# Performance work log

Hardware: AMD Instinct MI355X
Metric: run time of the kernel (lower is better)

Reference implementation:

```python
import jax, jax.numpy as jnp
import numpy as np

N = 50000
E_RAND = 800000
IN, HID, OUT = 128, 64, 40
HEADS = (2, 1, 1)
NEG_SLOPE = 0.2


def setup_inputs() -> dict:
    key = jax.random.key(0)
    ks = jax.random.split(key, 16)
    # random edges with src != dst, then append self-loops (remove+add_self_loop)
    src_r = jax.random.randint(ks[0], (E_RAND,), 0, N)
    off = jax.random.randint(ks[1], (E_RAND,), 1, N)
    dst_r = (src_r + off) % N
    loops = jnp.arange(N)
    src = jnp.concatenate([src_r, loops]).astype(jnp.int64)
    dst = jnp.concatenate([dst_r, loops]).astype(jnp.int64)
    in_feat = jax.random.normal(ks[2], (N, IN), dtype=jnp.float32)

    def lin(k, fan_in, fan_out):
        return jax.random.normal(k, (fan_in, fan_out), dtype=jnp.float32) / np.sqrt(fan_in)

    H0, H1, H2 = HEADS
    # layer 0: in=IN, out=HID, heads=H0
    W0 = lin(ks[3], IN, H0 * HID)
    al0 = jax.random.normal(ks[4], (H0, HID), dtype=jnp.float32) * 0.1
    ar0 = jax.random.normal(ks[5], (H0, HID), dtype=jnp.float32) * 0.1
    b0 = jnp.zeros((H0 * HID,), dtype=jnp.float32)
    # layer 1: in=HID*H0, out=HID, heads=H1
    W1 = lin(ks[6], HID * H0, H1 * HID)
    al1 = jax.random.normal(ks[7], (H1, HID), dtype=jnp.float32) * 0.1
    ar1 = jax.random.normal(ks[8], (H1, HID), dtype=jnp.float32) * 0.1
    b1 = jnp.zeros((H1 * HID,), dtype=jnp.float32)
    # layer 2: in=HID*H1, out=OUT, heads=H2
    W2 = lin(ks[9], HID * H1, H2 * OUT)
    al2 = jax.random.normal(ks[10], (H2, OUT), dtype=jnp.float32) * 0.1
    ar2 = jax.random.normal(ks[11], (H2, OUT), dtype=jnp.float32) * 0.1
    b2 = jnp.zeros((H2 * OUT,), dtype=jnp.float32)
    return {"in_feat": in_feat, "src": src, "dst": dst,
            "W0": W0, "al0": al0, "ar0": ar0, "b0": b0,
            "W1": W1, "al1": al1, "ar1": ar1, "b1": b1,
            "W2": W2, "al2": al2, "ar2": ar2, "b2": b2}


def _gat_layer(x, src, dst, W, al, ar, b):
    # x: [N, Fin]; W: [Fin, H*D]; al/ar: [H, D]; b: [H*D]
    H, D = al.shape
    feat = (x @ W).reshape(-1, H, D)                 # [N, H, D]
    el = jnp.sum(feat * al, axis=-1)                 # [N, H]
    er = jnp.sum(feat * ar, axis=-1)                 # [N, H]
    e = jax.nn.leaky_relu(el[src] + er[dst], NEG_SLOPE)  # [E, H]
    m = jax.ops.segment_max(e, dst, num_segments=x.shape[0])
    ee = jnp.exp(e - jax.lax.stop_gradient(m)[dst])
    s = jax.ops.segment_sum(ee, dst, num_segments=x.shape[0])
    alpha = ee / s[dst]                              # softmax over in-edges per dst
    out = jax.ops.segment_sum(feat[src] * alpha[:, :, None], dst,
                              num_segments=x.shape[0])  # [N, H, D]
    return out + b.reshape(1, H, D)


def reference(in_feat, src, dst, W0, al0, ar0, b0, W1, al1, ar1, b1, W2, al2, ar2, b2):
    h = _gat_layer(in_feat, src, dst, W0, al0, ar0, b0).reshape(in_feat.shape[0], -1)  # flatten(1)
    h = _gat_layer(h, src, dst, W1, al1, ar1, b1).mean(axis=1)                          # mean over heads
    h = _gat_layer(h, src, dst, W2, al2, ar2, b2).reshape(in_feat.shape[0], -1)         # flatten(1)
    return h
```

## Files before the change

### kernel.cpp

```cpp
#include <hip/hip_runtime.h>
#include <hip/hip_fp16.h>
#include <math.h>

#define NEG_SLOPE 0.2f

typedef _Float16 h8 __attribute__((ext_vector_type(8)));
typedef float f4 __attribute__((ext_vector_type(4)));


__device__ inline float2 up2(unsigned u) {
    __half2 h;
    __builtin_memcpy(&h, &u, 4);
    return __half22float2(h);
}
__device__ inline unsigned pk2(float a, float b) {
    __half2 h = __floats2half2_rn(a, b);
    unsigned u;
    __builtin_memcpy(&u, &h, 4);
    return u;
}
__device__ inline void fma8(float* acc, const uint4& v, float p) {
    float2 f;
    f = up2(v.x); acc[0] += f.x * p; acc[1] += f.y * p;
    f = up2(v.y); acc[2] += f.x * p; acc[3] += f.y * p;
    f = up2(v.z); acc[4] += f.x * p; acc[5] += f.y * p;
    f = up2(v.w); acc[6] += f.x * p; acc[7] += f.y * p;
}
__device__ inline float dot4(const float4& a, const float4& b) {
    return a.x * b.x + a.y * b.y + a.z * b.z + a.w * b.w;
}


__global__ __launch_bounds__(256) void prep(const float* __restrict__ W0,
                                            const float* __restrict__ W1,
                                            const float* __restrict__ W2,
                                            const float* __restrict__ al2,
                                            const float* __restrict__ ar2,
                                            __half* __restrict__ P0,
                                            __half* __restrict__ P1,
                                            __half* __restrict__ P2,
                                            float* __restrict__ al2p,
                                            float* __restrict__ ar2p,
                                            int* __restrict__ deg, int N) {
    int b = blockIdx.x;
    int gtid = b * 256 + threadIdx.x;
    for (int i = gtid; i < N; i += gridDim.x * 256) deg[i] = 0;

    if (b < 14) {
        const float* W;
        __half* P;
        int K, M, Msrc, lb = b;
        if (lb < 8) {
            W = W0; P = P0; K = 128; M = 128; Msrc = 128;
        } else if (lb < 12) {
            W = W1; P = P1; K = 128; M = 64; Msrc = 64; lb -= 8;
        } else {
            W = W2; P = P2; K = 64; M = 64; Msrc = 40; lb -= 12;
        }
        int t = lb * 256 + threadIdx.x;
        int nk8 = K >> 3;
        if (t < M * nk8) {
            int m = t % M, k8 = t / M;
            int k = k8 * 8;
            int c = m >> 4, s = k >> 5, hi = (k >> 3) & 3, lane = hi * 16 + (m & 15);
            float v[8];
#pragma unroll
            for (int i = 0; i < 8; ++i)
                v[i] = (m < Msrc) ? W[(size_t)(k + i) * Msrc + m] : 0.f;
            uint4 o;
            o.x = pk2(v[0], v[1]);
            o.y = pk2(v[2], v[3]);
            o.z = pk2(v[4], v[5]);
            o.w = pk2(v[6], v[7]);
            *(uint4*)(P + (size_t)((c * (K >> 5) + s) * 64 + lane) * 8) = o;
        }
    } else if (b == 14) {
        int t = threadIdx.x;
        if (t < 64) {
            al2p[t] = (t < 40) ? al2[t] : 0.f;
            ar2p[t] = (t < 40) ? ar2[t] : 0.f;
        }
    }
}


__global__ __launch_bounds__(256) void degree_hist_rank(const int* __restrict__ dst,
                                                        int* __restrict__ deg,
                                                        int* __restrict__ rank, int E) {
    int e = blockIdx.x * blockDim.x + threadIdx.x;
    if (e >= E) return;
    int d = __builtin_nontemporal_load(&dst[e]);
    int r = atomicAdd(&deg[d], 1);
    __builtin_nontemporal_store(r, &rank[e]);
}

__global__ __launch_bounds__(256) void scan_block_sums(const int* __restrict__ in,
                                                       int* __restrict__ partial, int n) {
    int i = blockIdx.x * 256 + threadIdx.x;
    int v = (i < n) ? in[i] : 0;
#pragma unroll
    for (int off = 32; off; off >>= 1) v += __shfl_xor(v, off);
    __shared__ int wsum[4];
    if ((threadIdx.x & 63) == 0) wsum[threadIdx.x >> 6] = v;
    __syncthreads();
    if (threadIdx.x == 0) partial[blockIdx.x] = wsum[0] + wsum[1] + wsum[2] + wsum[3];
}

__global__ __launch_bounds__(256) void scan_final2(const int* __restrict__ in,
                                                   const int* __restrict__ partial,
                                                   int* __restrict__ out, int n) {
    __shared__ int buf[256];
    __shared__ int wsum[4];
    int t = threadIdx.x;
    int i = blockIdx.x * 256 + t;
    int v = (i < n) ? in[i] : 0;
    buf[t] = v;
    __syncthreads();
    for (int off = 1; off < 256; off <<= 1) {
        int x = (t >= off) ? buf[t - off] : 0;
        __syncthreads();
        buf[t] += x;
        __syncthreads();
    }
    int incl = buf[t];
    int pv = (t < blockIdx.x) ? partial[t] : 0;
#pragma unroll
    for (int off = 32; off; off >>= 1) pv += __shfl_xor(pv, off);
    if ((t & 63) == 0) wsum[t >> 6] = pv;
    __syncthreads();
    int pre = wsum[0] + wsum[1] + wsum[2] + wsum[3];
    if (i < n) out[i] = pre + incl - v;
    if (i == n - 1) out[n] = pre + incl;
}

__global__ __launch_bounds__(256) void scatter_rank(const int* __restrict__ src,
                                                    const int* __restrict__ dst,
                                                    const int* __restrict__ rank,
                                                    const int* __restrict__ row_start,
                                                    int* __restrict__ csr_src, int E) {
    int e = blockIdx.x * blockDim.x + threadIdx.x;
    if (e >= E) return;
    int d = __builtin_nontemporal_load(&dst[e]);
    int s = __builtin_nontemporal_load(&src[e]);
    int r = __builtin_nontemporal_load(&rank[e]);
    csr_src[row_start[d] + r] = s;
}


template <int K, int M, int H, bool A16>
__global__ __launch_bounds__(256) void gemm_mfma(const void* __restrict__ xin,
                                                 const __half* __restrict__ Wp,
                                                 const float* __restrict__ al,
                                                 const float* __restrict__ ar,
                                                 __half* __restrict__ outh,
                                                 float* __restrict__ el,
                                                 float* __restrict__ er, int N) {
    constexpr int KS = K / 32;
    constexpr int CF = M / 16;
    constexpr int LDT = 133;
    constexpr int CH8 = M / 8;
    constexpr int NC8 = CH8 / 4;
    __shared__ float tl[4 * 16 * LDT];
    const int tid = threadIdx.x;
    const int wid = tid >> 6, lane = tid & 63;
    const int lhi = lane >> 4, llo = lane & 15;
    const int rowbase = blockIdx.x * 64 + wid * 16;
    float* wt = tl + wid * 16 * LDT;

    f4 acc[CF];
#pragma unroll
    for (int c = 0; c < CF; ++c) acc[c] = f4{0.f, 0.f, 0.f, 0.f};

    const int arow = rowbase + llo;
    const bool aval = arow < N;
#pragma unroll
    for (int s = 0; s < KS; ++s) {
        h8 a = {};
        if (aval) {
            if constexpr (A16) {
                const __half* xp = (const __half*)xin + (size_t)arow * K + s * 32 + lhi * 8;
                a = *(const h8*)xp;
            } else {
                const float4* xp = (const float4*)((const float*)xin + (size_t)arow * K +
                                                   s * 32 + lhi * 8);
                float4 x0 = xp[0];
                float4 x1 = xp[1];
                a[0] = (_Float16)x0.x; a[1] = (_Float16)x0.y;
                a[2] = (_Float16)x0.z; a[3] = (_Float16)x0.w;
                a[4] = (_Float16)x1.x; a[5] = (_Float16)x1.y;
                a[6] = (_Float16)x1.z; a[7] = (_Float16)x1.w;
            }
        }
#pragma unroll
        for (int c = 0; c < CF; ++c) {
            h8 b = *(const h8*)(Wp + (size_t)((c * KS + s) * 64 + lane) * 8);
            acc[c] = __builtin_amdgcn_mfma_f32_16x16x32_f16(a, b, acc[c], 0, 0, 0);
        }
    }

#pragma unroll
    for (int c = 0; c < CF; ++c) {
#pragma unroll
        for (int r = 0; r < 4; ++r)
            wt[(lhi * 4 + r) * LDT + c * 16 + llo] = acc[c][r];
    }

    const int rrow = lane >> 2;
    const int q = lane & 3;
    const int grow = rowbase + rrow;
    float elp[H], erp[H];
#pragma unroll
    for (int h = 0; h < H; ++h) { elp[h] = 0.f; erp[h] = 0.f; }
    const float4* al4 = (const float4*)al;
    const float4* ar4 = (const float4*)ar;
#pragma unroll
    for (int i = 0; i < NC8; ++i) {
        int j8 = q + 4 * i;
        float4 v0 = *(float4*)&wt[rrow * LDT + 8 * j8];
        float4 v1 = *(float4*)&wt[rrow * LDT + 8 * j8 + 4];
        int h = (H == 2 && i >= NC8 / 2) ? 1 : 0;
        float4 a0 = al4[2 * j8], a1 = al4[2 * j8 + 1];
        float4 r0 = ar4[2 * j8], r1 = ar4[2 * j8 + 1];
        elp[h] += dot4(v0, a0) + dot4(v1, a1);
        erp[h] += dot4(v0, r0) + dot4(v1, r1);
        if (grow < N) {
            uint4 pkv;
            pkv.x = pk2(v0.x, v0.y);
            pkv.y = pk2(v0.z, v0.w);
            pkv.z = pk2(v1.x, v1.y);
            pkv.w = pk2(v1.z, v1.w);
            *(uint4*)(outh + (size_t)grow * M + 8 * j8) = pkv;
        }
    }
#pragma unroll
    for (int h = 0; h < H; ++h) {
#pragma unroll
        for (int off = 1; off < 4; off <<= 1) {
            elp[h] += __shfl_xor(elp[h], off);
            erp[h] += __shfl_xor(erp[h], off);
        }
    }
    if (q == 0 && grow < N) {
        if constexpr (H == 2) {
            *(float2*)&el[(size_t)grow * 2] = float2{elp[0], elp[1]};
            *(float2*)&er[(size_t)grow * 2] = float2{erp[0], erp[1]};
        } else {
            el[grow] = elp[0];
            er[grow] = erp[0];
        }
    }
}


template <int H, int D, int FSTRIDE, int T, bool OUT16>
__global__ __launch_bounds__(256) void gat_aggregate3(const __half* __restrict__ feat,
                                                      const float* __restrict__ el,
                                                      const float* __restrict__ er,
                                                      const int* __restrict__ row_start,
                                                      const int* __restrict__ csr_src,
                                                      const float* __restrict__ bias,
                                                      void* __restrict__ out, int N) {
    constexpr int NLp = FSTRIDE / 8;
    constexpr int GnH = 32 / NLp;
    constexpr int BATCH = GnH * T;
    constexpr int WL = (H * D) / 8;
    static_assert(32 % NLp == 0 && BATCH == 32, "whole trip in one round");
    int pair = (blockIdx.x * blockDim.x + threadIdx.x) >> 6;
    int lane = threadIdx.x & 63;
    if (pair * 2 >= N) return;
    const int l32 = lane & 31;
    const int hb = lane & 32;
    const int dstn = pair * 2 + (lane >> 5);
    const bool dval = dstn < N;
    int beg = dval ? row_start[dstn] : 0;
    int end = dval ? row_start[dstn + 1] : 0;
    int cnt = end - beg;

    float er_d[H];
#pragma unroll
    for (int h = 0; h < H; ++h) er_d[h] = dval ? er[(size_t)dstn * H + h] : 0.f;

    float ssum[H];
    float acc8[8];
#pragma unroll
    for (int h = 0; h < H; ++h) ssum[h] = 0.f;
#pragma unroll
    for (int i = 0; i < 8; ++i) acc8[i] = 0.f;

    const int g = l32 / NLp;
    const int ln = l32 % NLp;
    const uint4* fp = (const uint4*)feat;

    int trips = (cnt + 31) >> 5;
    {
        int to = __shfl_xor(trips, 32);
        trips = (to > trips) ? to : trips;
    }

    for (int it = 0; it < trips; ++it) {
        int base = beg + it * 32;
        int idx = base + l32;
        bool valid = idx < end;
        int s = csr_src[valid ? idx : beg];
        int cc = end - base;
        cc = (cc < 0) ? 0 : ((cc > 32) ? 32 : cc);

        float ev0 = 0.f, ev1 = 0.f;
        if constexpr (H == 2) {
            float2 e2 = ((const float2*)el)[s];
            ev0 = e2.x;
            ev1 = e2.y;
        } else {
            ev0 = el[s];
        }

        uint4 v[T];
#pragma unroll
        for (int t = 0; t < T; ++t) {
            if (GnH * t < cc) {
                int sj = __shfl(s, hb + GnH * t + g);
                v[t] = fp[(size_t)sj * NLp + ln];
            }
        }

        float p[H];
        if constexpr (H == 2) {
            float e0 = ev0 + er_d[0];
            float e1 = ev1 + er_d[1];
            e0 = (e0 > 0.f) ? e0 : NEG_SLOPE * e0;
            e1 = (e1 > 0.f) ? e1 : NEG_SLOPE * e1;
            p[0] = valid ? __expf(e0) : 0.f;
            p[1] = valid ? __expf(e1) : 0.f;
            ssum[0] += p[0];
            ssum[1] += p[1];
        } else {
            float e = ev0 + er_d[0];
            e = (e > 0.f) ? e : NEG_SLOPE * e;
            p[0] = valid ? __expf(e) : 0.f;
            ssum[0] += p[0];
        }

#pragma unroll
        for (int t = 0; t < T; ++t) {
            if (GnH * t < cc) {
                int slot = hb + GnH * t + g;
                float pj = __shfl(p[0], slot);
                if constexpr (H == 2) {
                    float pj1 = __shfl(p[1], slot);
                    pj = (ln >= 8) ? pj1 : pj;
                }
                fma8(acc8, v[t], pj);
            }
        }
    }

#pragma unroll
    for (int h = 0; h < H; ++h)
#pragma unroll
        for (int off = 16; off; off >>= 1) ssum[h] += __shfl_xor(ssum[h], off);
#pragma unroll
    for (int i = 0; i < 8; ++i) {
#pragma unroll
        for (int off = NLp; off < 32; off <<= 1) acc8[i] += __shfl_xor(acc8[i], off);
    }
    if (l32 < WL && dval) {
        float inv;
        if constexpr (H == 2) inv = 1.f / ((l32 >= 8) ? ssum[1] : ssum[0]);
        else inv = 1.f / ssum[0];
        const float4* bp = (const float4*)bias;
        float4 bv0 = bp[2 * l32], bv1 = bp[2 * l32 + 1];
        float4 o0, o1;
        o0.x = acc8[0] * inv + bv0.x; o0.y = acc8[1] * inv + bv0.y;
        o0.z = acc8[2] * inv + bv0.z; o0.w = acc8[3] * inv + bv0.w;
        o1.x = acc8[4] * inv + bv1.x; o1.y = acc8[5] * inv + bv1.y;
        o1.z = acc8[6] * inv + bv1.z; o1.w = acc8[7] * inv + bv1.w;
        if constexpr (OUT16) {
            __half* op = (__half*)out + (size_t)dstn * (H * D);
            uint4 pkv;
            pkv.x = pk2(o0.x, o0.y);
            pkv.y = pk2(o0.z, o0.w);
            pkv.z = pk2(o1.x, o1.y);
            pkv.w = pk2(o1.z, o1.w);
            ((uint4*)op)[l32] = pkv;
        } else {
            float4* op = (float4*)((float*)out + (size_t)dstn * (H * D));
            op[2 * l32] = o0;
            op[2 * l32 + 1] = o1;
        }
    }
}


extern "C" void kernel_launch(void* const* d_in, const int* in_sizes, int n_in,
                              void* d_out, int out_size, void* d_ws, size_t ws_size,
                              hipStream_t stream) {
    const float* in_feat = (const float*)d_in[0];
    const int*   src     = (const int*)d_in[1];
    const int*   dst     = (const int*)d_in[2];
    const float* W0 = (const float*)d_in[3];
    const float* al0 = (const float*)d_in[4];
    const float* ar0 = (const float*)d_in[5];
    const float* b0 = (const float*)d_in[6];
    const float* W1 = (const float*)d_in[7];
    const float* al1 = (const float*)d_in[8];
    const float* ar1 = (const float*)d_in[9];
    const float* b1 = (const float*)d_in[10];
    const float* W2 = (const float*)d_in[11];
    const float* al2 = (const float*)d_in[12];
    const float* ar2 = (const float*)d_in[13];
    const float* b2 = (const float*)d_in[14];
    float* out = (float*)d_out;

    const int N = in_sizes[0] / 128;
    const int E = in_sizes[1];

    char* ws = (char*)d_ws;
    auto alloc = [&](size_t bytes) -> void* {
        void* p = (void*)ws;
        ws += (bytes + 255) & ~(size_t)255;
        return p;
    };
    int* deg       = (int*)alloc((size_t)N * 4);
    int* row_start = (int*)alloc((size_t)(N + 1) * 4);
    int* csr_src   = (int*)alloc((size_t)E * 4);
    int* rank      = (int*)alloc((size_t)E * 4);
    int* partial   = (int*)alloc(256 * 4);
    __half* feat   = (__half*)alloc((size_t)N * 128 * 2);
    float* el      = (float*)alloc((size_t)N * 2 * 4);
    float* er      = (float*)alloc((size_t)N * 2 * 4);
    __half* h0h    = (__half*)alloc((size_t)N * 128 * 2);
    __half* h1h    = (__half*)alloc((size_t)N * 64 * 2);
    __half* Wp0    = (__half*)alloc((size_t)128 * 128 * 2);
    __half* Wp1    = (__half*)alloc((size_t)128 * 64 * 2);
    __half* Wp2    = (__half*)alloc((size_t)64 * 64 * 2);
    float* al2p    = (float*)alloc(64 * 4);
    float* ar2p    = (float*)alloc(64 * 4);

    int egrid = (E + 255) / 256;
    int nb = (N + 255) / 256;

    prep<<<256, 256, 0, stream>>>(W0, W1, W2, al2, ar2, Wp0, Wp1, Wp2, al2p, ar2p, deg, N);
    degree_hist_rank<<<egrid, 256, 0, stream>>>(dst, deg, rank, E);
    scan_block_sums<<<nb, 256, 0, stream>>>(deg, partial, N);
    scan_final2<<<nb, 256, 0, stream>>>(deg, partial, row_start, N);
    scatter_rank<<<egrid, 256, 0, stream>>>(src, dst, rank, row_start, csr_src, E);

    int npairs = (N + 1) / 2;
    int pgrid = (npairs * 64 + 255) / 256;
    int mgrid = (N + 63) / 64;

    gemm_mfma<128, 128, 2, false><<<mgrid, 256, 0, stream>>>(in_feat, Wp0, al0, ar0, feat, el, er, N);
    gat_aggregate3<2, 64, 128, 16, true><<<pgrid, 256, 0, stream>>>(feat, el, er, row_start, csr_src, b0, h0h, N);

    gemm_mfma<128, 64, 1, true><<<mgrid, 256, 0, stream>>>(h0h, Wp1, al1, ar1, feat, el, er, N);
    gat_aggregate3<1, 64, 64, 8, true><<<pgrid, 256, 0, stream>>>(feat, el, er, row_start, csr_src, b1, h1h, N);

    gemm_mfma<64, 64, 1, true><<<mgrid, 256, 0, stream>>>(h1h, Wp2, al2p, ar2p, feat, el, er, N);
    gat_aggregate3<1, 40, 64, 8, false><<<pgrid, 256, 0, stream>>>(feat, el, er, row_start, csr_src, b2, out, N);
}
```

Measured before the change: 264.5 us.

## Merge scan passes into one kernel and fuse CSR scatter with layer-0 GEMM

Replaces the two-pass block scan with a single kernel in which each block recomputes its prefix by summing every earlier degree entry directly. The CSR scatter is fused with the first-layer MFMA GEMM in one launch, and the first ntiles blocks also run the GEMM tile. The aim is to cut two kernel launches and their serialization gaps. The cost is redundant reads of deg in the scan (up to about N per block, quadratic overall but small) and the scatter blocks carrying large shared memory, which may lower occupancy.

Measured after the change: 282.7 us. +6.9%, slower.

```diff
diff --git a/kernel.cpp b/kernel.cpp
--- a/kernel.cpp
+++ b/kernel.cpp
@@ -94,26 +94,14 @@
     __builtin_nontemporal_store(r, &rank[e]);
 }
 
-__global__ __launch_bounds__(256) void scan_block_sums(const int* __restrict__ in,
-                                                       int* __restrict__ partial, int n) {
-    int i = blockIdx.x * 256 + threadIdx.x;
-    int v = (i < n) ? in[i] : 0;
-#pragma unroll
-    for (int off = 32; off; off >>= 1) v += __shfl_xor(v, off);
-    __shared__ int wsum[4];
-    if ((threadIdx.x & 63) == 0) wsum[threadIdx.x >> 6] = v;
-    __syncthreads();
-    if (threadIdx.x == 0) partial[blockIdx.x] = wsum[0] + wsum[1] + wsum[2] + wsum[3];
-}
-
-__global__ __launch_bounds__(256) void scan_final2(const int* __restrict__ in,
-                                                   const int* __restrict__ partial,
-                                                   int* __restrict__ out, int n) {
+__global__ __launch_bounds__(256) void scan_one(const int* __restrict__ deg,
+                                                int* __restrict__ out, int n) {
     __shared__ int buf[256];
     __shared__ int wsum[4];
     int t = threadIdx.x;
-    int i = blockIdx.x * 256 + t;
-    int v = (i < n) ? in[i] : 0;
+    int b = blockIdx.x;
+    int i = b * 256 + t;
+    int v = (i < n) ? deg[i] : 0;
     buf[t] = v;
     __syncthreads();
     for (int off = 1; off < 256; off <<= 1) {
@@ -123,7 +111,8 @@
         __syncthreads();
     }
     int incl = buf[t];
-    int pv = (t < blockIdx.x) ? partial[t] : 0;
+    int pv = 0;
+    for (int j = t; j < b * 256; j += 256) pv += deg[j];
 #pragma unroll
     for (int off = 32; off; off >>= 1) pv += __shfl_xor(pv, off);
     if ((t & 63) == 0) wsum[t >> 6] = pv;
@@ -133,39 +122,21 @@
     if (i == n - 1) out[n] = pre + incl;
 }
 
-__global__ __launch_bounds__(256) void scatter_rank(const int* __restrict__ src,
-                                                    const int* __restrict__ dst,
-                                                    const int* __restrict__ rank,
-                                                    const int* __restrict__ row_start,
-                                                    int* __restrict__ csr_src, int E) {
-    int e = blockIdx.x * blockDim.x + threadIdx.x;
-    if (e >= E) return;
-    int d = __builtin_nontemporal_load(&dst[e]);
-    int s = __builtin_nontemporal_load(&src[e]);
-    int r = __builtin_nontemporal_load(&rank[e]);
-    csr_src[row_start[d] + r] = s;
-}
-
 
 template <int K, int M, int H, bool A16>
-__global__ __launch_bounds__(256) void gemm_mfma(const void* __restrict__ xin,
-                                                 const __half* __restrict__ Wp,
-                                                 const float* __restrict__ al,
-                                                 const float* __restrict__ ar,
-                                                 __half* __restrict__ outh,
-                                                 float* __restrict__ el,
-                                                 float* __restrict__ er, int N) {
+__device__ __forceinline__ void dev_gemm(float* wt, const void* __restrict__ xin,
+                                         const __half* __restrict__ Wp,
+                                         const float* __restrict__ al,
+                                         const float* __restrict__ ar,
+                                         __half* __restrict__ outh,
+                                         float* __restrict__ el,
+                                         float* __restrict__ er, int rowbase, int N) {
     constexpr int KS = K / 32;
     constexpr int CF = M / 16;
     constexpr int LDT = 133;
-    constexpr int CH8 = M / 8;
-    constexpr int NC8 = CH8 / 4;
-    __shared__ float tl[4 * 16 * LDT];
-    const int tid = threadIdx.x;
-    const int wid = tid >> 6, lane = tid & 63;
+    constexpr int NC8 = (M / 8) / 4;
+    const int lane = threadIdx.x & 63;
     const int lhi = lane >> 4, llo = lane & 15;
-    const int rowbase = blockIdx.x * 64 + wid * 16;
-    float* wt = tl + wid * 16 * LDT;
 
     f4 acc[CF];
 #pragma unroll
@@ -248,6 +219,44 @@
             el[grow] = elp[0];
             er[grow] = erp[0];
         }
+    }
+}
+
+template <int K, int M, int H, bool A16>
+__global__ __launch_bounds__(256) void gemm_mfma(const void* __restrict__ xin,
+                                                 const __half* __restrict__ Wp,
+                                                 const float* __restrict__ al,
+                                                 const float* __restrict__ ar,
+                                                 __half* __restrict__ outh,
+                                                 float* __restrict__ el,
+                                                 float* __restrict__ er, int N) {
+    __shared__ float tl[4 * 16 * 133];
+    const int wid = threadIdx.x >> 6;
+    dev_gemm<K, M, H, A16>(tl + wid * 16 * 133, xin, Wp, al, ar, outh, el, er,
+                           blockIdx.x * 64 + wid * 16, N);
+}
+
+__global__ __launch_bounds__(256) void scatter_gemm0(
+    const int* __restrict__ src, const int* __restrict__ dst,
+    const int* __restrict__ rank, const int* __restrict__ row_start,
+    int* __restrict__ csr_src,
+    const float* __restrict__ in_feat, const __half* __restrict__ Wp0,
+    const float* __restrict__ al0, const float* __restrict__ ar0,
+    __half* __restrict__ feat0, float* __restrict__ el0, float* __restrict__ er0,
+    int N, int E) {
+    __shared__ float tl[4 * 16 * 133];
+    int e = blockIdx.x * 256 + threadIdx.x;
+    if (e < E) {
+        int d = __builtin_nontemporal_load(&dst[e]);
+        int s = __builtin_nontemporal_load(&src[e]);
+        int r = __builtin_nontemporal_load(&rank[e]);
+        csr_src[row_start[d] + r] = s;
+    }
+    const int ntiles = (N + 63) >> 6;
+    if (blockIdx.x < ntiles) {
+        const int wid = threadIdx.x >> 6;
+        dev_gemm<128, 128, 2, false>(tl + wid * 16 * 133, in_feat, Wp0, al0, ar0,
+                                     feat0, el0, er0, blockIdx.x * 64 + wid * 16, N);
     }
 }
 
@@ -424,7 +433,6 @@
     int* row_start = (int*)alloc((size_t)(N + 1) * 4);
     int* csr_src   = (int*)alloc((size_t)E * 4);
     int* rank      = (int*)alloc((size_t)E * 4);
-    int* partial   = (int*)alloc(256 * 4);
     __half* feat   = (__half*)alloc((size_t)N * 128 * 2);
     float* el      = (float*)alloc((size_t)N * 2 * 4);
     float* er      = (float*)alloc((size_t)N * 2 * 4);
@@ -441,15 +449,14 @@
 
     prep<<<256, 256, 0, stream>>>(W0, W1, W2, al2, ar2, Wp0, Wp1, Wp2, al2p, ar2p, deg, N);
     degree_hist_rank<<<egrid, 256, 0, stream>>>(dst, deg, rank, E);
-    scan_block_sums<<<nb, 256, 0, stream>>>(deg, partial, N);
-    scan_final2<<<nb, 256, 0, stream>>>(deg, partial, row_start, N);
-    scatter_rank<<<egrid, 256, 0, stream>>>(src, dst, rank, row_start, csr_src, E);
+    scan_one<<<nb, 256, 0, stream>>>(deg, row_start, N);
+    scatter_gemm0<<<egrid, 256, 0, stream>>>(src, dst, rank, row_start, csr_src,
+                                             in_feat, Wp0, al0, ar0, feat, el, er, N, E);
 
     int npairs = (N + 1) / 2;
     int pgrid = (npairs * 64 + 255) / 256;
     int mgrid = (N + 63) / 64;
 
-    gemm_mfma<128, 128, 2, false><<<mgrid, 256, 0, stream>>>(in_feat, Wp0, al0, ar0, feat, el, er, N);
     gat_aggregate3<2, 64, 128, 16, true><<<pgrid, 256, 0, stream>>>(feat, el, er, row_start, csr_src, b0, h0h, N);
 
     gemm_mfma<128, 64, 1, true><<<mgrid, 256, 0, stream>>>(h0h, Wp1, al1, ar1, feat, el, er, N);
```
